# Optimization experiments

Measured on AMD Instinct MI355X. Metric: run time of the kernel, lower is better.

Reference implementation:

```python
import jax, jax.numpy as jnp
import numpy as np

# Human3.6M skeleton: 16 bones over 17 joints
SKELETON = [(0,1),(1,2),(2,3),(0,4),(4,5),(5,6),(0,7),(7,8),(8,9),(9,10),(8,11),(11,12),(12,13),(8,14),(14,15),(15,16)]
PARENT = jnp.array([p for p, c in SKELETON], dtype=jnp.int32)
CHILD = jnp.array([c for p, c in SKELETON], dtype=jnp.int32)
NUM_BONES = 16
EPS = 1e-9


def setup_inputs() -> dict:
    key = jax.random.key(0)
    k1, k2, k3, k4, k5 = jax.random.split(key, 5)
    B, J = 1000000, 17
    pred_jts = jax.random.normal(k1, (B, J, 3), dtype=jnp.float32)
    gt_bl = jax.random.uniform(k2, (B, NUM_BONES), dtype=jnp.float32)
    anchor_scores = jax.random.uniform(k3, (B, J), dtype=jnp.float32)
    # ShiftAttention params: fc1 (32->16), fc2 (16->32), no bias; stored as [in, out]
    W1 = jax.random.normal(k4, (2 * NUM_BONES, NUM_BONES), dtype=jnp.float32) * (2.0 / (2 * NUM_BONES)) ** 0.5
    W2 = jax.random.normal(k5, (NUM_BONES, 2 * NUM_BONES), dtype=jnp.float32) * (2.0 / NUM_BONES) ** 0.5
    return {"pred_jts": pred_jts, "gt_bl": gt_bl, "anchor_scores": anchor_scores, "W1": W1, "W2": W2}


def reference(pred_jts, gt_bl, anchor_scores, W1, W2):
    B = pred_jts.shape[0]
    # per-edge gather: bone vectors [B, 16, 3]
    diff = pred_jts[:, PARENT, :] - pred_jts[:, CHILD, :]
    bl_norm = jnp.linalg.norm(diff, axis=-1)            # [B, 16]
    dis_bl = gt_bl - bl_norm                            # bone-length error
    a_p = anchor_scores[:, PARENT]
    a_c = anchor_scores[:, CHILD]
    a_sum = a_p + a_c + EPS
    # split correction between parent (weighted by child score) and child
    move_bl = jnp.stack([dis_bl * a_c / a_sum, dis_bl * a_p / a_sum], axis=-1)  # [B, 16, 2]
    # ShiftAttention gate: sigmoid(relu(x W1) W2)
    x = move_bl.reshape(B, 2 * NUM_BONES)
    gate = jax.nn.sigmoid(jax.nn.relu(x @ W1) @ W2).reshape(B, NUM_BONES, 2)
    move_bl = move_bl * gate
    # unit bone directions and per-edge forces
    unit = diff / (bl_norm[..., None] + EPS)            # [B, 16, 3]
    force_parent = move_bl[..., 0:1] * unit
    force_child = -move_bl[..., 1:2] * unit
    # scatter-add forces into joints (duplicate joint indices accumulate)
    move_jts = jnp.zeros_like(pred_jts).at[:, PARENT].add(force_parent).at[:, CHILD].add(force_child)
    return pred_jts + move_jts
```

## Files before the change

kernel.cpp:

```cpp
#include <hip/hip_runtime.h>

#define DEV __device__ __forceinline__

typedef __fp16 h16x2 __attribute__((ext_vector_type(2)));

DEV void gload_lds16(const void* g, void* lds) {
    __builtin_amdgcn_global_load_lds(
        (const __attribute__((address_space(1))) void*)g,
        (__attribute__((address_space(3))) void*)lds,
        16, 0, 0);
}

DEV float dot2(h16x2 a, h16x2 b, float acc) {
    asm("v_dot2_f32_f16 %0, %1, %2, %0" : "+v"(acc) : "v"(a), "v"(b));
    return acc;
}

DEV h16x2 f2h(float a, float b) { return __builtin_amdgcn_cvt_pkrtz(a, b); }

DEV float fast_sigmoid(float v) {
    return __builtin_amdgcn_rcpf(1.0f + __builtin_amdgcn_exp2f(-1.4426950408889634f * v));
}

DEV void compute_sample(const float (&p)[51], const float (&a)[17], const float (&g)[16],
                        const float4* sW1h4, const float4* sW2h4, float (&o)[51])
{
    constexpr int PAR[16] = {0,1,2,0,4,5,0,7,8,9,8,11,12,8,14,15};
    constexpr int CHI[16] = {1,2,3,4,5,6,7,8,9,10,11,12,13,14,15,16};

    float x[32], invn[16];
    #pragma unroll
    for (int k = 0; k < 16; ++k) {
        const int P = PAR[k] * 3, C = CHI[k] * 3;
        const float dx = p[P]   - p[C];
        const float dy = p[P+1] - p[C+1];
        const float dz = p[P+2] - p[C+2];
        const float n  = __builtin_amdgcn_sqrtf(fmaf(dx,dx, fmaf(dy,dy, dz*dz)));
        const float dis = g[k] - n;
        const float ap = a[PAR[k]], ac = a[CHI[k]];
        const float inv_asum = __builtin_amdgcn_rcpf(ap + ac + 1e-9f);
        x[2*k]   = dis * ac * inv_asum;
        x[2*k+1] = dis * ap * inv_asum;
        invn[k]  = __builtin_amdgcn_rcpf(n + 1e-9f);
    }

    h16x2 xp[16];
    #pragma unroll
    for (int ip = 0; ip < 16; ++ip) xp[ip] = f2h(x[2*ip], x[2*ip+1]);

    float y[16];
    #pragma unroll
    for (int j = 0; j < 16; ++j) y[j] = 0.f;
    #pragma unroll
    for (int ip = 0; ip < 16; ++ip) {
        #pragma unroll
        for (int jj = 0; jj < 4; ++jj) {
            const float4 wq = sW1h4[ip*4 + jj];
            y[4*jj+0] = dot2(xp[ip], __builtin_bit_cast(h16x2, wq.x), y[4*jj+0]);
            y[4*jj+1] = dot2(xp[ip], __builtin_bit_cast(h16x2, wq.y), y[4*jj+1]);
            y[4*jj+2] = dot2(xp[ip], __builtin_bit_cast(h16x2, wq.z), y[4*jj+2]);
            y[4*jj+3] = dot2(xp[ip], __builtin_bit_cast(h16x2, wq.w), y[4*jj+3]);
        }
    }
    h16x2 hp[8];
    #pragma unroll
    for (int jp = 0; jp < 8; ++jp)
        hp[jp] = f2h(fmaxf(y[2*jp], 0.f), fmaxf(y[2*jp+1], 0.f));

    float gg[32];
    #pragma unroll
    for (int c = 0; c < 32; ++c) gg[c] = 0.f;
    #pragma unroll
    for (int jp = 0; jp < 8; ++jp) {
        #pragma unroll
        for (int cc = 0; cc < 8; ++cc) {
            const float4 wq = sW2h4[jp*8 + cc];
            gg[4*cc+0] = dot2(hp[jp], __builtin_bit_cast(h16x2, wq.x), gg[4*cc+0]);
            gg[4*cc+1] = dot2(hp[jp], __builtin_bit_cast(h16x2, wq.y), gg[4*cc+1]);
            gg[4*cc+2] = dot2(hp[jp], __builtin_bit_cast(h16x2, wq.z), gg[4*cc+2]);
            gg[4*cc+3] = dot2(hp[jp], __builtin_bit_cast(h16x2, wq.w), gg[4*cc+3]);
        }
    }

    float xg[32];
    #pragma unroll
    for (int c = 0; c < 32; ++c) xg[c] = x[c] * fast_sigmoid(gg[c]);
    #pragma unroll
    for (int k = 0; k < 16; ++k) {
        xg[2*k]   *= invn[k];
        xg[2*k+1] *= invn[k];
    }

    #pragma unroll
    for (int j = 0; j < 17; ++j) {
        float ox = p[3*j], oy = p[3*j+1], oz = p[3*j+2];
        #pragma unroll
        for (int k = 0; k < 16; ++k) {
            if (PAR[k] == j || CHI[k] == j) {
                const int P = PAR[k] * 3, C = CHI[k] * 3;
                const float dx = p[P]   - p[C];
                const float dy = p[P+1] - p[C+1];
                const float dz = p[P+2] - p[C+2];
                const float s = (PAR[k] == j) ? xg[2*k] : -xg[2*k+1];
                ox = fmaf(s, dx, ox);
                oy = fmaf(s, dy, oy);
                oz = fmaf(s, dz, oz);
            }
        }
        o[3*j]   = ox;
        o[3*j+1] = oy;
        o[3*j+2] = oz;
    }
}

__global__ __launch_bounds__(256, 2) void projts_kernel(
    const float* __restrict__ pred,
    const float* __restrict__ gt,
    const float* __restrict__ anc,
    const float* __restrict__ gW1,
    const float* __restrict__ gW2,
    float* __restrict__ out,
    int B)
{
    constexpr int ROW = 51;
    constexpr int WBUF = 64 * ROW;

    __shared__ h16x2 sW1h[256] __attribute__((aligned(16)));
    __shared__ h16x2 sW2h[256] __attribute__((aligned(16)));
    __shared__ float sbuf[4][WBUF] __attribute__((aligned(16)));

    const int t = threadIdx.x;

    {
        const int ip = t >> 4, j = t & 15;
        sW1h[t] = f2h(gW1[32*ip + j], gW1[32*ip + 16 + j]);
        const int jp = t >> 5, c = t & 31;
        sW2h[t] = f2h(gW2[64*jp + c], gW2[64*jp + 32 + c]);
    }
    __syncthreads();

    const float4* sW1h4 = reinterpret_cast<const float4*>(sW1h);
    const float4* sW2h4 = reinterpret_cast<const float4*>(sW2h);

    const int w = t >> 6;
    const int l = t & 63;

    if ((long long)(blockIdx.x + 1) * 256 <= (long long)B) {
        const long long wavebase = ((long long)blockIdx.x * 4 + w) * 64;
        float* buf  = sbuf[w];
        float4* buf4 = reinterpret_cast<float4*>(buf);
        float p[51], a[17], o[51];

        const char* srcB = reinterpret_cast<const char*>(pred + (size_t)wavebase * ROW);
        char* bufB = reinterpret_cast<char*>(buf);

        #pragma unroll
        for (int i = 0; i < 12; ++i)
            gload_lds16(srcB + (size_t)(i*64 + l)*16, bufB + i*1024);
        if (l < 48)
            gload_lds16(srcB + (size_t)(768 + l)*16, bufB + 12*1024);

        const float4* asrc4 = reinterpret_cast<const float4*>(anc + (size_t)wavebase * 17);
        float4 ar0 = asrc4[0*64 + l];
        float4 ar1 = asrc4[1*64 + l];
        float4 ar2 = asrc4[2*64 + l];
        float4 ar3 = asrc4[3*64 + l];
        float4 ar4 = asrc4[256 + (l & 15)];

        const float4* gsrc4 = reinterpret_cast<const float4*>(gt + (size_t)(wavebase + l) * 16);
        const float4 gq0 = gsrc4[0], gq1 = gsrc4[1], gq2 = gsrc4[2], gq3 = gsrc4[3];

        __syncthreads();

        #pragma unroll
        for (int j = 0; j < ROW; ++j) p[j] = buf[l*ROW + j];

        __syncthreads();

        buf4[0*64 + l] = ar0;
        buf4[1*64 + l] = ar1;
        buf4[2*64 + l] = ar2;
        buf4[3*64 + l] = ar3;
        buf4[256 + l]  = ar4;

        __syncthreads();

        #pragma unroll
        for (int j = 0; j < 17; ++j) a[j] = buf[l*17 + j];

        __syncthreads();

        const float g[16] = {gq0.x,gq0.y,gq0.z,gq0.w, gq1.x,gq1.y,gq1.z,gq1.w,
                             gq2.x,gq2.y,gq2.z,gq2.w, gq3.x,gq3.y,gq3.z,gq3.w};

        compute_sample(p, a, g, sW1h4, sW2h4, o);

        #pragma unroll
        for (int j = 0; j < ROW; ++j) buf[l*ROW + j] = o[j];

        __syncthreads();

        float4* dst4 = reinterpret_cast<float4*>(out + (size_t)wavebase * ROW);
        #pragma unroll
        for (int i = 0; i < 12; ++i) dst4[i*64 + l] = buf4[i*64 + l];
        if (l < 48) dst4[768 + l] = buf4[768 + l];
    } else {
        const long long b = (long long)blockIdx.x * 256 + t;
        if (b < B) {
            float p[51], a[17], g[16], o[51];
            const float* pj = pred + (size_t)b * 51;
            #pragma unroll
            for (int j = 0; j < 51; ++j) p[j] = pj[j];
            const float* ab = anc + (size_t)b * 17;
            #pragma unroll
            for (int j = 0; j < 17; ++j) a[j] = ab[j];
            const float* gb = gt + (size_t)b * 16;
            #pragma unroll
            for (int j = 0; j < 16; ++j) g[j] = gb[j];

            compute_sample(p, a, g, sW1h4, sW2h4, o);

            float* ob = out + (size_t)b * 51;
            #pragma unroll
            for (int j = 0; j < 51; ++j) ob[j] = o[j];
        }
    }
}

extern "C" void kernel_launch(void* const* d_in, const int* in_sizes, int n_in,
                              void* d_out, int out_size, void* d_ws, size_t ws_size,
                              hipStream_t stream) {
    const float* pred = (const float*)d_in[0];
    const float* gt   = (const float*)d_in[1];
    const float* anc  = (const float*)d_in[2];
    const float* W1   = (const float*)d_in[3];
    const float* W2   = (const float*)d_in[4];
    float* out = (float*)d_out;

    const int B = in_sizes[0] / 51;
    const int blocks = (B + 255) / 256;
    hipLaunchKernelGGL(projts_kernel, dim3(blocks), dim3(256), 0, stream,
                       pred, gt, anc, W1, W2, out, B);
}
```

Before: 113.4 us.

## Stage fp16 weights inside per-wave LDS buffer and drop dedicated weight arrays

Removes the block-wide shared fp16 weight arrays and the prologue that filled them and synchronised before any input loads. Each wave now loads and packs the weights itself after its joint tile has been read, writing them into an unused region of its own staging buffer. This cuts static LDS per block, which may allow a third block per CU, and lets the input prefetch start immediately. The tail path now computes the MLP in fp32 directly from global weights. The cost is redundant weight loads and packing in every wave.

```diff
diff --git a/kernel.cpp b/kernel.cpp
--- a/kernel.cpp
+++ b/kernel.cpp
@@ -22,11 +22,14 @@
     return __builtin_amdgcn_rcpf(1.0f + __builtin_amdgcn_exp2f(-1.4426950408889634f * v));
 }
 
+#define SKEL_TABLES \
+    constexpr int PAR[16] = {0,1,2,0,4,5,0,7,8,9,8,11,12,8,14,15}; \
+    constexpr int CHI[16] = {1,2,3,4,5,6,7,8,9,10,11,12,13,14,15,16};
+
 DEV void compute_sample(const float (&p)[51], const float (&a)[17], const float (&g)[16],
                         const float4* sW1h4, const float4* sW2h4, float (&o)[51])
 {
-    constexpr int PAR[16] = {0,1,2,0,4,5,0,7,8,9,8,11,12,8,14,15};
-    constexpr int CHI[16] = {1,2,3,4,5,6,7,8,9,10,11,12,13,14,15,16};
+    SKEL_TABLES
 
     float x[32], invn[16];
     #pragma unroll
@@ -113,6 +116,80 @@
     }
 }
 
+DEV void compute_sample_f32(const float (&p)[51], const float (&a)[17], const float (&g)[16],
+                            const float* __restrict__ gW1, const float* __restrict__ gW2,
+                            float (&o)[51])
+{
+    SKEL_TABLES
+
+    float x[32], invn[16];
+    #pragma unroll
+    for (int k = 0; k < 16; ++k) {
+        const int P = PAR[k] * 3, C = CHI[k] * 3;
+        const float dx = p[P]   - p[C];
+        const float dy = p[P+1] - p[C+1];
+        const float dz = p[P+2] - p[C+2];
+        const float n  = __builtin_amdgcn_sqrtf(fmaf(dx,dx, fmaf(dy,dy, dz*dz)));
+        const float dis = g[k] - n;
+        const float ap = a[PAR[k]], ac = a[CHI[k]];
+        const float inv_asum = __builtin_amdgcn_rcpf(ap + ac + 1e-9f);
+        x[2*k]   = dis * ac * inv_asum;
+        x[2*k+1] = dis * ap * inv_asum;
+        invn[k]  = __builtin_amdgcn_rcpf(n + 1e-9f);
+    }
+
+    float y[16];
+    #pragma unroll
+    for (int j = 0; j < 16; ++j) y[j] = 0.f;
+    for (int i = 0; i < 32; ++i) {
+        const float xi = x[i];
+        #pragma unroll
+        for (int j = 0; j < 16; ++j) y[j] = fmaf(xi, gW1[i*16 + j], y[j]);
+    }
+    float h[16];
+    #pragma unroll
+    for (int j = 0; j < 16; ++j) h[j] = fmaxf(y[j], 0.f);
+
+    float gg[32];
+    #pragma unroll
+    for (int c = 0; c < 32; ++c) gg[c] = 0.f;
+    for (int j = 0; j < 16; ++j) {
+        const float hj = h[j];
+        #pragma unroll
+        for (int c = 0; c < 32; ++c) gg[c] = fmaf(hj, gW2[j*32 + c], gg[c]);
+    }
+
+    float xg[32];
+    #pragma unroll
+    for (int c = 0; c < 32; ++c) xg[c] = x[c] * fast_sigmoid(gg[c]);
+    #pragma unroll
+    for (int k = 0; k < 16; ++k) {
+        xg[2*k]   *= invn[k];
+        xg[2*k+1] *= invn[k];
+    }
+
+    #pragma unroll
+    for (int j = 0; j < 17; ++j) {
+        float ox = p[3*j], oy = p[3*j+1], oz = p[3*j+2];
+        #pragma unroll
+        for (int k = 0; k < 16; ++k) {
+            if (PAR[k] == j || CHI[k] == j) {
+                const int P = PAR[k] * 3, C = CHI[k] * 3;
+                const float dx = p[P]   - p[C];
+                const float dy = p[P+1] - p[C+1];
+                const float dz = p[P+2] - p[C+2];
+                const float s = (PAR[k] == j) ? xg[2*k] : -xg[2*k+1];
+                ox = fmaf(s, dx, ox);
+                oy = fmaf(s, dy, oy);
+                oz = fmaf(s, dz, oz);
+            }
+        }
+        o[3*j]   = ox;
+        o[3*j+1] = oy;
+        o[3*j+2] = oz;
+    }
+}
+
 __global__ __launch_bounds__(256, 2) void projts_kernel(
     const float* __restrict__ pred,
     const float* __restrict__ gt,
@@ -124,31 +201,20 @@
 {
     constexpr int ROW = 51;
     constexpr int WBUF = 64 * ROW;
-
-    __shared__ h16x2 sW1h[256] __attribute__((aligned(16)));
-    __shared__ h16x2 sW2h[256] __attribute__((aligned(16)));
+    constexpr int WOFF1 = 1536;
+    constexpr int WOFF2 = 1792;
+
     __shared__ float sbuf[4][WBUF] __attribute__((aligned(16)));
 
     const int t = threadIdx.x;
-
-    {
-        const int ip = t >> 4, j = t & 15;
-        sW1h[t] = f2h(gW1[32*ip + j], gW1[32*ip + 16 + j]);
-        const int jp = t >> 5, c = t & 31;
-        sW2h[t] = f2h(gW2[64*jp + c], gW2[64*jp + 32 + c]);
-    }
-    __syncthreads();
-
-    const float4* sW1h4 = reinterpret_cast<const float4*>(sW1h);
-    const float4* sW2h4 = reinterpret_cast<const float4*>(sW2h);
-
     const int w = t >> 6;
     const int l = t & 63;
 
+    float* buf  = sbuf[w];
+    float4* buf4 = reinterpret_cast<float4*>(buf);
+
     if ((long long)(blockIdx.x + 1) * 256 <= (long long)B) {
         const long long wavebase = ((long long)blockIdx.x * 4 + w) * 64;
-        float* buf  = sbuf[w];
-        float4* buf4 = reinterpret_cast<float4*>(buf);
         float p[51], a[17], o[51];
 
         const char* srcB = reinterpret_cast<const char*>(pred + (size_t)wavebase * ROW);
@@ -170,6 +236,18 @@
         const float4* gsrc4 = reinterpret_cast<const float4*>(gt + (size_t)(wavebase + l) * 16);
         const float4 gq0 = gsrc4[0], gq1 = gsrc4[1], gq2 = gsrc4[2], gq3 = gsrc4[3];
 
+        float w1a[4], w1b[4], w2a[4], w2b[4];
+        #pragma unroll
+        for (int q = 0; q < 4; ++q) {
+            const int t4 = l + 64*q;
+            const int ip = t4 >> 4, j = t4 & 15;
+            w1a[q] = gW1[32*ip + j];
+            w1b[q] = gW1[32*ip + 16 + j];
+            const int jp = t4 >> 5, c = t4 & 31;
+            w2a[q] = gW2[64*jp + c];
+            w2b[q] = gW2[64*jp + 32 + c];
+        }
+
         __syncthreads();
 
         #pragma unroll
@@ -182,6 +260,11 @@
         buf4[2*64 + l] = ar2;
         buf4[3*64 + l] = ar3;
         buf4[256 + l]  = ar4;
+        #pragma unroll
+        for (int q = 0; q < 4; ++q) {
+            buf[WOFF1 + l + 64*q] = __builtin_bit_cast(float, f2h(w1a[q], w1b[q]));
+            buf[WOFF2 + l + 64*q] = __builtin_bit_cast(float, f2h(w2a[q], w2b[q]));
+        }
 
         __syncthreads();
 
@@ -193,6 +276,8 @@
         const float g[16] = {gq0.x,gq0.y,gq0.z,gq0.w, gq1.x,gq1.y,gq1.z,gq1.w,
                              gq2.x,gq2.y,gq2.z,gq2.w, gq3.x,gq3.y,gq3.z,gq3.w};
 
+        const float4* sW1h4 = reinterpret_cast<const float4*>(buf + WOFF1);
+        const float4* sW2h4 = reinterpret_cast<const float4*>(buf + WOFF2);
         compute_sample(p, a, g, sW1h4, sW2h4, o);
 
         #pragma unroll
@@ -218,7 +303,7 @@
             #pragma unroll
             for (int j = 0; j < 16; ++j) g[j] = gb[j];
 
-            compute_sample(p, a, g, sW1h4, sW2h4, o);
+            compute_sample_f32(p, a, g, gW1, gW2, o);
 
             float* ob = out + (size_t)b * 51;
             #pragma unroll
```

Result: faster. 107.6 us (-5.1%).
